# Kernel optimization log

Hardware: AMD Instinct MI355X
Metric: run time of the kernel (lower is better)

The kernel has to match this reference:

```python
import jax, jax.numpy as jnp
import numpy as np

ETYPES = [0, 2, 1]          # indexes into doubled RotatE0 r_vec (2*R rows)
OUT_DIM = 64
NUM_HEADS = 8
ALPHA = 0.01                # LeakyReLU slope
R = 2                       # raw relation count (r_vec rows before doubling)
N = 100000                  # num nodes
E = 250000                  # num edges (metapath instances)
L = len(ETYPES) + 1         # metapath length


def setup_inputs() -> dict:
    key = jax.random.key(0)
    k = jax.random.split(key, 6)
    features = jax.random.normal(k[0], (N, OUT_DIM), jnp.float32)
    r_vec = jax.random.normal(k[1], (R, OUT_DIM // 2, 2), jnp.float32)
    attn1_w = jax.random.normal(k[2], (NUM_HEADS, OUT_DIM), jnp.float32) * 0.1
    attn2 = jax.random.normal(k[3], (1, NUM_HEADS, OUT_DIM), jnp.float32) * 0.1
    edge_metapath_indices = jax.random.randint(k[4], (E, L), 0, N)
    edge_dst = jax.random.randint(k[5], (E,), 0, N)
    return {"features": features, "r_vec": r_vec, "attn1_w": attn1_w,
            "attn2": attn2, "edge_metapath_indices": edge_metapath_indices,
            "edge_dst": edge_dst}


def _forward(features, r_vec, attn1_w, attn2, edge_metapath_indices, edge_dst):
    D2 = OUT_DIM // 2
    # --- RotatE0 relation vectors: normalize each complex pair to unit length ---
    rv = r_vec / jnp.linalg.norm(r_vec, axis=2, keepdims=True)      # [R, D2, 2]
    rv_conj = rv * jnp.array([1.0, -1.0], rv.dtype)                 # conjugate
    rv2 = jnp.stack((rv, rv_conj), axis=1).reshape(2 * R, D2, 2)    # [2R, D2, 2]
    # --- cumulative rotation per metapath position (reverse product) ---
    fr = [None] * L
    fr[L - 1] = jnp.stack([jnp.ones(D2, rv.dtype), jnp.zeros(D2, rv.dtype)], -1)
    for i in range(L - 2, -1, -1):
        if ETYPES[i] is not None:
            r = rv2[ETYPES[i]]                                       # [D2, 2]
            re = fr[i + 1][:, 0] * r[:, 0] - fr[i + 1][:, 1] * r[:, 1]
            im = fr[i + 1][:, 0] * r[:, 1] + fr[i + 1][:, 1] * r[:, 0]
            fr[i] = jnp.stack([re, im], axis=-1)
        else:
            fr[i] = fr[i + 1]
    frv = jnp.stack(fr, axis=0)                                      # [L, D2, 2]
    # --- gather node features along each metapath instance ---
    edata = features[edge_metapath_indices]                          # [E, L, D]
    ed = edata.reshape(edata.shape[0], L, D2, 2)
    # position L-1 has identity rotation (1,0), so rotate all positions at once
    re = ed[..., 0] * frv[None, :, :, 0] - ed[..., 1] * frv[None, :, :, 1]
    im = ed[..., 0] * frv[None, :, :, 1] + ed[..., 1] * frv[None, :, :, 0]
    ed = jnp.stack([re, im], axis=-1).reshape(edata.shape[0], L, OUT_DIM)
    hidden = ed.mean(axis=1)                                         # [E, D]
    eft = jnp.tile(hidden, (1, NUM_HEADS)).reshape(-1, NUM_HEADS, OUT_DIM)
    # --- attention scores (attn_switch=True) ---
    center = features[edge_metapath_indices[:, -1]]                  # [E, D]
    a1 = center @ attn1_w.T                                          # [E, H]
    a2 = (eft * attn2).sum(axis=-1)                                  # [E, H]
    a = a1 + a2
    a = jnp.where(a > 0, a, ALPHA * a)[:, :, None]                   # leaky relu, [E,H,1]
    # --- edge softmax over destination-node segments ---
    amax = jax.lax.stop_gradient(jax.ops.segment_max(a, edge_dst, num_segments=N))
    aexp = jnp.exp(a - amax[edge_dst])
    asum = jax.ops.segment_sum(aexp, edge_dst, num_segments=N)
    attn = aexp / asum[edge_dst]                                     # [E, H, 1]
    # --- message passing: weighted scatter-sum to destination nodes ---
    h = jax.ops.segment_sum(eft * attn, edge_dst, num_segments=N)    # [N, H, D]
    return h


def reference(features, r_vec, attn1_w, attn2, edge_metapath_indices, edge_dst):
    return _forward(features, r_vec, attn1_w, attn2, edge_metapath_indices, edge_dst)
```

## Files before the change

### kernel.cpp

```cpp
#include <hip/hip_runtime.h>

#define NUM_HEADS 8

__device__ __forceinline__ float2 cmul(float2 a, float2 b) {
    return make_float2(a.x*b.x - a.y*b.y, a.x*b.y + a.y*b.x);
}

__global__ __launch_bounds__(256) void k_pre(
    const float4* __restrict__ feat4,
    const float2* __restrict__ rvec,
    const float2* __restrict__ w1_g,
    const float2* __restrict__ w2_g,
    float*        __restrict__ P, int N)
{
    __shared__ float4 sf[1024];
    int tid = threadIdx.x;
    int lane = tid & 31;
    int l = lane >> 3, h = lane & 7;

    float2 Wr[32];
    for (int d = 0; d < 32; ++d) {
        float2 a = rvec[d], b = rvec[32 + d];
        float na = rsqrtf(a.x*a.x + a.y*a.y); a.x *= na; a.y *= na;
        float nb = rsqrtf(b.x*b.x + b.y*b.y); b.x *= nb; b.y *= nb;
        float2 fr2 = make_float2(a.x, -a.y);
        float2 fr1 = cmul(fr2, b);
        float2 fr0 = cmul(fr1, a);
        float2 fr = (l == 0) ? fr0 : (l == 1) ? fr1 : (l == 2) ? fr2 : make_float2(1.f, 0.f);
        float2 frc = make_float2(fr.x, -fr.y);
        float2 w2 = w2_g[h*32 + d];
        float2 wl = cmul(w2, frc);
        wl.x *= 0.25f; wl.y *= 0.25f;
        if (l == 3) { float2 w1 = w1_g[h*32 + d]; wl.x += w1.x; wl.y += w1.y; }
        Wr[d] = wl;
    }

    int n0 = blockIdx.x * 64;
    int lim = (N - n0) * 16;
    for (int i = tid; i < 1024; i += 256)
        sf[i] = (i < lim) ? feat4[(size_t)n0 * 16 + i] : make_float4(0.f, 0.f, 0.f, 0.f);
    __syncthreads();

    int grp = tid >> 5;
    #pragma unroll
    for (int k = 0; k < 8; ++k) {
        int n = n0 + grp * 8 + k;
        if (n >= N) break;
        const float4* fp = &sf[(grp * 8 + k) * 16];
        float acc = 0.f;
        #pragma unroll
        for (int q = 0; q < 16; ++q) {
            float4 v = fp[q];
            acc += v.x * Wr[2*q].x + v.y * Wr[2*q].y
                 + v.z * Wr[2*q+1].x + v.w * Wr[2*q+1].y;
        }
        P[(size_t)n * 32 + lane] = acc;
    }
}

__global__ void k_count(const int* __restrict__ edge_dst, int* __restrict__ counts, int E) {
    int e = blockIdx.x * 256 + threadIdx.x;
    if (e < E) atomicAdd(&counts[edge_dst[e]], 1);
}

__global__ __launch_bounds__(256) void k_scan_a(
    const int* __restrict__ counts, int* __restrict__ offsets,
    int* __restrict__ blocksums, int N)
{
    __shared__ int s[256];
    int t = threadIdx.x;
    int base = blockIdx.x * 1024 + t * 4;
    int v0 = (base     < N) ? counts[base]     : 0;
    int v1 = (base + 1 < N) ? counts[base + 1] : 0;
    int v2 = (base + 2 < N) ? counts[base + 2] : 0;
    int v3 = (base + 3 < N) ? counts[base + 3] : 0;
    s[t] = v0 + v1 + v2 + v3;
    __syncthreads();
    #pragma unroll
    for (int off = 1; off < 256; off <<= 1) {
        int x = (t >= off) ? s[t - off] : 0;
        __syncthreads();
        s[t] += x;
        __syncthreads();
    }
    if (t == 255) blocksums[blockIdx.x] = s[255];
    int run = (t == 0) ? 0 : s[t - 1];
    if (base     < N) offsets[base]     = run; run += v0;
    if (base + 1 < N) offsets[base + 1] = run; run += v1;
    if (base + 2 < N) offsets[base + 2] = run; run += v2;
    if (base + 3 < N) offsets[base + 3] = run;
}

__global__ __launch_bounds__(1024) void k_scan_b(
    int* __restrict__ blocksums, int* __restrict__ total, int B)
{
    __shared__ int s[1024];
    int t = threadIdx.x;
    s[t] = (t < B) ? blocksums[t] : 0;
    __syncthreads();
    #pragma unroll
    for (int off = 1; off < 1024; off <<= 1) {
        int x = (t >= off) ? s[t - off] : 0;
        __syncthreads();
        s[t] += x;
        __syncthreads();
    }
    if (t < B) blocksums[t] = (t == 0) ? 0 : s[t - 1];
    if (t == 1023) *total = s[1023];
}

__global__ __launch_bounds__(256) void k_scan_c(
    int* __restrict__ offsets, int* __restrict__ cursor,
    const int* __restrict__ blocksums, const int* __restrict__ total, int N)
{
    int i = blockIdx.x * 256 + threadIdx.x;
    if (i < N) {
        int v = offsets[i] + blocksums[i >> 10];
        offsets[i] = v;
        cursor[i] = v;
    }
    if (i == 0) offsets[N] = *total;
}

__global__ __launch_bounds__(256) void k_edge(
    const float2* __restrict__ feat,
    const float2* __restrict__ rvec,
    const float*  __restrict__ P,
    const int4*   __restrict__ emi,
    const int*    __restrict__ edge_dst,
    int*          __restrict__ cursor,
    float2*       __restrict__ hbuf,
    int E)
{
    __shared__ float2 s_frv[96];
    int tid = threadIdx.x;
    if (tid < 32) {
        float2 a = rvec[tid], b = rvec[32 + tid];
        float na = rsqrtf(a.x*a.x + a.y*a.y); a.x *= na; a.y *= na;
        float nb = rsqrtf(b.x*b.x + b.y*b.y); b.x *= nb; b.y *= nb;
        float2 fr2 = make_float2(a.x, -a.y);
        float2 fr1 = cmul(fr2, b);
        float2 fr0 = cmul(fr1, a);
        s_frv[tid] = fr0; s_frv[32 + tid] = fr1; s_frv[64 + tid] = fr2;
    }
    __syncthreads();

    int e = blockIdx.x * 8 + (tid >> 5);
    if (e >= E) return;
    int lane = tid & 31;

    int4 idx = emi[e];
    int pos = 0;
    if (lane == 0) pos = atomicAdd(&cursor[edge_dst[e]], 1);
    pos = __shfl(pos, 0, 32);

    float2 f0 = feat[(size_t)idx.x * 32 + lane];
    float2 f1 = feat[(size_t)idx.y * 32 + lane];
    float2 f2 = feat[(size_t)idx.z * 32 + lane];
    float2 c3 = feat[(size_t)idx.w * 32 + lane];
    float2 fr0 = s_frv[lane], fr1 = s_frv[32 + lane], fr2 = s_frv[64 + lane];

    float2 hv;
    hv.x = c3.x + f0.x*fr0.x - f0.y*fr0.y
                + f1.x*fr1.x - f1.y*fr1.y
                + f2.x*fr2.x - f2.y*fr2.y;
    hv.y = c3.y + f0.x*fr0.y + f0.y*fr0.x
                + f1.x*fr1.y + f1.y*fr1.x
                + f2.x*fr2.y + f2.y*fr2.x;
    hv.x *= 0.25f; hv.y *= 0.25f;

    float2* row = hbuf + (size_t)pos * 36;
    row[lane] = hv;

    if (lane < NUM_HEADS) {
        float a = P[(size_t)idx.x * 32 + lane]
                + P[(size_t)idx.y * 32 +  8 + lane]
                + P[(size_t)idx.z * 32 + 16 + lane]
                + P[(size_t)idx.w * 32 + 24 + lane];
        a = a > 0.f ? a : 0.01f * a;
        ((float*)(row + 32))[lane] = __expf(a);
    }
}

__global__ __launch_bounds__(256) void k_out(
    const float2* __restrict__ hbuf,
    const int*    __restrict__ offsets,
    float2*       __restrict__ out,
    int N)
{
    int tid = threadIdx.x;
    int n = blockIdx.x * 8 + (tid >> 5);
    if (n >= N) return;
    int lane = tid & 31;
    int beg = offsets[n], end = offsets[n + 1];

    if (beg == end) {
        float2 z = make_float2(0.f, 0.f);
        #pragma unroll
        for (int hh = 0; hh < NUM_HEADS; ++hh)
            out[((size_t)n * 8 + hh) * 32 + lane] = z;
        return;
    }

    float dsum[NUM_HEADS];
    float2 acc[NUM_HEADS];
    #pragma unroll
    for (int hh = 0; hh < NUM_HEADS; ++hh) { dsum[hh] = 0.f; acc[hh] = make_float2(0.f, 0.f); }

    for (int j = beg; j < end; ++j) {
        const float2* row = hbuf + (size_t)j * 36;
        float2 hv = row[lane];
        float4 wa = ((const float4*)(row + 32))[0];
        float4 wb = ((const float4*)(row + 32))[1];
        dsum[0] += wa.x; acc[0].x += wa.x * hv.x; acc[0].y += wa.x * hv.y;
        dsum[1] += wa.y; acc[1].x += wa.y * hv.x; acc[1].y += wa.y * hv.y;
        dsum[2] += wa.z; acc[2].x += wa.z * hv.x; acc[2].y += wa.z * hv.y;
        dsum[3] += wa.w; acc[3].x += wa.w * hv.x; acc[3].y += wa.w * hv.y;
        dsum[4] += wb.x; acc[4].x += wb.x * hv.x; acc[4].y += wb.x * hv.y;
        dsum[5] += wb.y; acc[5].x += wb.y * hv.x; acc[5].y += wb.y * hv.y;
        dsum[6] += wb.z; acc[6].x += wb.z * hv.x; acc[6].y += wb.z * hv.y;
        dsum[7] += wb.w; acc[7].x += wb.w * hv.x; acc[7].y += wb.w * hv.y;
    }

    #pragma unroll
    for (int hh = 0; hh < NUM_HEADS; ++hh) {
        float r = 1.f / dsum[hh];
        out[((size_t)n * 8 + hh) * 32 + lane] = make_float2(acc[hh].x * r, acc[hh].y * r);
    }
}

extern "C" void kernel_launch(void* const* d_in, const int* in_sizes, int n_in,
                              void* d_out, int out_size, void* d_ws, size_t ws_size,
                              hipStream_t stream) {
    const float2* feat = (const float2*)d_in[0];
    const float2* rvec = (const float2*)d_in[1];
    const float2* w1   = (const float2*)d_in[2];
    const float2* w2   = (const float2*)d_in[3];
    const int4*   emi  = (const int4*)d_in[4];
    const int* edge_dst = (const int*)d_in[5];

    int N = in_sizes[0] / 64;
    int E = in_sizes[4] / 4;
    int nTiles = (N + 1023) / 1024;

    char* w = (char*)d_ws;
    float*  P        = (float*)w;
    float2* hbuf     = (float2*)(P + (size_t)N * 32);
    int*    counts   = (int*)(hbuf + (size_t)E * 36);
    int*    offsets  = counts + N;
    int*    cursor   = offsets + N + 1;
    int*    blocksums= cursor + N;
    int*    total    = blocksums + 1024;

    hipMemsetAsync(counts, 0, (size_t)N * 4, stream);

    k_count<<<(E + 255) / 256, 256, 0, stream>>>(edge_dst, counts, E);
    k_pre<<<(N + 63) / 64, 256, 0, stream>>>((const float4*)feat, rvec, w1, w2, P, N);
    k_scan_a<<<nTiles, 256, 0, stream>>>(counts, offsets, blocksums, N);
    k_scan_b<<<1, 1024, 0, stream>>>(blocksums, total, nTiles);
    k_scan_c<<<(N + 255) / 256, 256, 0, stream>>>(offsets, cursor, blocksums, total, N);
    k_edge<<<(E + 7) / 8, 256, 0, stream>>>(feat, rvec, P, emi, edge_dst, cursor,
                                            hbuf, E);
    k_out<<<(N + 7) / 8, 256, 0, stream>>>(hbuf, offsets, (float2*)d_out, N);
}
```

Measured before the change: 406.1 us.

## Store edge data in edge order and gather via sorted edge-id permutation

```diff
diff --git a/kernel.cpp b/kernel.cpp
--- a/kernel.cpp
+++ b/kernel.cpp
@@ -1,9 +1,16 @@
 #include <hip/hip_runtime.h>
 
 #define NUM_HEADS 8
+
+typedef float f2 __attribute__((ext_vector_type(2)));
 
 __device__ __forceinline__ float2 cmul(float2 a, float2 b) {
     return make_float2(a.x*b.x - a.y*b.y, a.x*b.y + a.y*b.x);
+}
+
+__device__ __forceinline__ void nt_store2(float2* p, float x, float y) {
+    f2 v; v.x = x; v.y = y;
+    __builtin_nontemporal_store(v, (f2*)p);
 }
 
 __global__ __launch_bounds__(256) void k_pre(
@@ -122,14 +129,21 @@
     if (i == 0) offsets[N] = *total;
 }
 
+__global__ void k_fill(const int* __restrict__ edge_dst, int* __restrict__ cursor,
+                       int* __restrict__ edge_ids, int E) {
+    int e = blockIdx.x * 256 + threadIdx.x;
+    if (e >= E) return;
+    int pos = atomicAdd(&cursor[edge_dst[e]], 1);
+    edge_ids[pos] = e;
+}
+
 __global__ __launch_bounds__(256) void k_edge(
     const float2* __restrict__ feat,
     const float2* __restrict__ rvec,
     const float*  __restrict__ P,
     const int4*   __restrict__ emi,
-    const int*    __restrict__ edge_dst,
-    int*          __restrict__ cursor,
-    float2*       __restrict__ hbuf,
+    float2*       __restrict__ hidden,
+    float*        __restrict__ w_buf,
     int E)
 {
     __shared__ float2 s_frv[96];
@@ -150,10 +164,6 @@
     int lane = tid & 31;
 
     int4 idx = emi[e];
-    int pos = 0;
-    if (lane == 0) pos = atomicAdd(&cursor[edge_dst[e]], 1);
-    pos = __shfl(pos, 0, 32);
-
     float2 f0 = feat[(size_t)idx.x * 32 + lane];
     float2 f1 = feat[(size_t)idx.y * 32 + lane];
     float2 f2 = feat[(size_t)idx.z * 32 + lane];
@@ -168,9 +178,7 @@
                 + f1.x*fr1.y + f1.y*fr1.x
                 + f2.x*fr2.y + f2.y*fr2.x;
     hv.x *= 0.25f; hv.y *= 0.25f;
-
-    float2* row = hbuf + (size_t)pos * 36;
-    row[lane] = hv;
+    hidden[(size_t)e * 32 + lane] = hv;
 
     if (lane < NUM_HEADS) {
         float a = P[(size_t)idx.x * 32 + lane]
@@ -178,13 +186,15 @@
                 + P[(size_t)idx.z * 32 + 16 + lane]
                 + P[(size_t)idx.w * 32 + 24 + lane];
         a = a > 0.f ? a : 0.01f * a;
-        ((float*)(row + 32))[lane] = __expf(a);
+        w_buf[(size_t)e * 8 + lane] = __expf(a);
     }
 }
 
 __global__ __launch_bounds__(256) void k_out(
-    const float2* __restrict__ hbuf,
+    const float2* __restrict__ hidden,
+    const float*  __restrict__ w_buf,
     const int*    __restrict__ offsets,
+    const int*    __restrict__ edge_ids,
     float2*       __restrict__ out,
     int N)
 {
@@ -195,10 +205,9 @@
     int beg = offsets[n], end = offsets[n + 1];
 
     if (beg == end) {
-        float2 z = make_float2(0.f, 0.f);
         #pragma unroll
         for (int hh = 0; hh < NUM_HEADS; ++hh)
-            out[((size_t)n * 8 + hh) * 32 + lane] = z;
+            nt_store2(&out[((size_t)n * 8 + hh) * 32 + lane], 0.f, 0.f);
         return;
     }
 
@@ -208,10 +217,10 @@
     for (int hh = 0; hh < NUM_HEADS; ++hh) { dsum[hh] = 0.f; acc[hh] = make_float2(0.f, 0.f); }
 
     for (int j = beg; j < end; ++j) {
-        const float2* row = hbuf + (size_t)j * 36;
-        float2 hv = row[lane];
-        float4 wa = ((const float4*)(row + 32))[0];
-        float4 wb = ((const float4*)(row + 32))[1];
+        int e = edge_ids[j];
+        const float4* wp = (const float4*)(w_buf + (size_t)e * 8);
+        float4 wa = wp[0], wb = wp[1];
+        float2 hv = hidden[(size_t)e * 32 + lane];
         dsum[0] += wa.x; acc[0].x += wa.x * hv.x; acc[0].y += wa.x * hv.y;
         dsum[1] += wa.y; acc[1].x += wa.y * hv.x; acc[1].y += wa.y * hv.y;
         dsum[2] += wa.z; acc[2].x += wa.z * hv.x; acc[2].y += wa.z * hv.y;
@@ -225,7 +234,7 @@
     #pragma unroll
     for (int hh = 0; hh < NUM_HEADS; ++hh) {
         float r = 1.f / dsum[hh];
-        out[((size_t)n * 8 + hh) * 32 + lane] = make_float2(acc[hh].x * r, acc[hh].y * r);
+        nt_store2(&out[((size_t)n * 8 + hh) * 32 + lane], acc[hh].x * r, acc[hh].y * r);
     }
 }
 
@@ -245,21 +254,25 @@
 
     char* w = (char*)d_ws;
     float*  P        = (float*)w;
-    float2* hbuf     = (float2*)(P + (size_t)N * 32);
-    int*    counts   = (int*)(hbuf + (size_t)E * 36);
+    float*  hidden   = P + (size_t)N * 32;
+    float*  w_buf    = hidden + (size_t)E * 64;
+    int*    counts   = (int*)(w_buf + (size_t)E * 8);
     int*    offsets  = counts + N;
     int*    cursor   = offsets + N + 1;
-    int*    blocksums= cursor + N;
+    int*    edge_ids = cursor + N;
+    int*    blocksums= edge_ids + E;
     int*    total    = blocksums + 1024;
 
-    hipMemsetAsync(counts, 0, (size_t)N * 4, stream);
+    (void)hipMemsetAsync(counts, 0, (size_t)N * 4, stream);
 
     k_count<<<(E + 255) / 256, 256, 0, stream>>>(edge_dst, counts, E);
     k_pre<<<(N + 63) / 64, 256, 0, stream>>>((const float4*)feat, rvec, w1, w2, P, N);
+    k_edge<<<(E + 7) / 8, 256, 0, stream>>>(feat, rvec, P, emi,
+                                            (float2*)hidden, w_buf, E);
     k_scan_a<<<nTiles, 256, 0, stream>>>(counts, offsets, blocksums, N);
     k_scan_b<<<1, 1024, 0, stream>>>(blocksums, total, nTiles);
     k_scan_c<<<(N + 255) / 256, 256, 0, stream>>>(offsets, cursor, blocksums, total, N);
-    k_edge<<<(E + 7) / 8, 256, 0, stream>>>(feat, rvec, P, emi, edge_dst, cursor,
-                                            hbuf, E);
-    k_out<<<(N + 7) / 8, 256, 0, stream>>>(hbuf, offsets, (float2*)d_out, N);
-}
+    k_fill<<<(E + 255) / 256, 256, 0, stream>>>(edge_dst, cursor, edge_ids, E);
+    k_out<<<(N + 7) / 8, 256, 0, stream>>>((const float2*)hidden, w_buf,
+                                           offsets, edge_ids, (float2*)d_out, N);
+}
```

Result: faster. 382.9 us (-5.7%).
